# Kernel optimization log

Hardware: AMD Instinct MI355X
Metric: run time of the kernel (lower is better)

The kernel has to match this reference:

```python
import jax, jax.numpy as jnp
import numpy as np

N = 100000   # nodes
E = 600000   # edges
F = 128      # input features
H = 128      # hidden size
A = 64       # n_actions
G = 64       # number of graphs in batch
L = 3        # GAT layers
EPS = 1e-5   # GraphNorm eps


def setup_inputs() -> dict:
    key = jax.random.key(0)
    ks = jax.random.split(key, 8)
    x = jax.random.normal(ks[0], (N, F), dtype=jnp.float32)
    edge_index = jax.random.randint(ks[1], (2, E), 0, N, dtype=jnp.int64)
    batch = jnp.sort(jax.random.randint(ks[2], (N,), 0, G, dtype=jnp.int64))
    Ws = jax.random.normal(ks[3], (L, H, H), dtype=jnp.float32) * (1.0 / np.sqrt(H))
    att_src = jax.random.normal(ks[4], (L, H), dtype=jnp.float32) * 0.1
    att_dst = jax.random.normal(ks[5], (L, H), dtype=jnp.float32) * 0.1
    conv_bias = jnp.zeros((L, H), dtype=jnp.float32)
    gn_weight = jnp.ones((L - 1, H), dtype=jnp.float32)
    gn_bias = jnp.zeros((L - 1, H), dtype=jnp.float32)
    gn_mean_scale = jnp.ones((L - 1, H), dtype=jnp.float32)
    W1 = jax.random.normal(ks[6], (H, H), dtype=jnp.float32) * (1.0 / np.sqrt(H))
    b1 = jnp.zeros((H,), dtype=jnp.float32)
    W2 = jax.random.normal(ks[7], (H, A), dtype=jnp.float32) * (1.0 / np.sqrt(H))
    b2 = jnp.zeros((A,), dtype=jnp.float32)
    return dict(x=x, edge_index=edge_index, batch=batch, Ws=Ws, att_src=att_src,
                att_dst=att_dst, conv_bias=conv_bias, gn_weight=gn_weight,
                gn_bias=gn_bias, gn_mean_scale=gn_mean_scale,
                W1=W1, b1=b1, W2=W2, b2=b2)


def reference(x, edge_index, batch, Ws, att_src, att_dst, conv_bias,
              gn_weight, gn_bias, gn_mean_scale, W1, b1, W2, b2):
    src, dst = edge_index[0], edge_index[1]
    n = x.shape[0]
    h = x
    for l in range(L):
        # GATConv (heads=1, add_self_loops=False): h' = W h, edge attention
        hW = h @ Ws[l]                              # [N,H]
        a_s = hW @ att_src[l]                       # [N]
        a_d = hW @ att_dst[l]                       # [N]
        e = jax.nn.leaky_relu(a_s[src] + a_d[dst], 0.2)      # [E]
        m = jax.ops.segment_max(e, dst, num_segments=n)      # stable softmax per dst
        ex = jnp.exp(e - m[dst])
        s = jax.ops.segment_sum(ex, dst, num_segments=n)
        alpha = ex / (s[dst] + 1e-16)               # PyG softmax eps
        h = jax.ops.segment_sum(hW[src] * alpha[:, None], dst, num_segments=n) + conv_bias[l]
        if l < L - 1:
            # GraphNorm with batch=None (source passes no batch to gnn): one graph
            mean = h.mean(axis=0, keepdims=True)
            out = h - mean * gn_mean_scale[l]
            var = (out * out).mean(axis=0, keepdims=True)
            h = gn_weight[l] * out / jnp.sqrt(var + EPS) + gn_bias[l]
            h = jax.nn.leaky_relu(h, 0.01)          # act between layers (not after last)
    pooled = jax.ops.segment_sum(h, batch, num_segments=G)   # global_add_pool [G,H]
    z = jax.nn.leaky_relu(pooled @ W1 + b1, 0.01)
    return z @ W2 + b2                               # [G,A]
```

## Files before the change

kernel.cpp:

```cpp
#include <hip/hip_runtime.h>
#include <math.h>

#define HD 128
#define GG 64
#define CSB 256

typedef __attribute__((ext_vector_type(8))) short short8;
typedef __attribute__((ext_vector_type(4))) float f32x4;
typedef __attribute__((ext_vector_type(2))) float f32x2;

__device__ __forceinline__ float leaky(float x, float s) { return x > 0.f ? x : s * x; }

__device__ __forceinline__ unsigned short bf16_of(float f) {
    union { float f; unsigned u; } v; v.f = f;
    unsigned r = v.u + 0x7fffu + ((v.u >> 16) & 1u);
    return (unsigned short)(r >> 16);
}
__device__ __forceinline__ float f_of_bf16(unsigned short u) {
    union { unsigned u; float f; } v; v.u = ((unsigned)u) << 16;
    return v.f;
}

__device__ __forceinline__ int sw(int row, int chunk) {
    return row * 128 + ((chunk ^ (row & 15)) << 3);
}

__global__ void k_init(const float* __restrict__ Ws, unsigned short* __restrict__ Wt,
                       int* __restrict__ bcnt) {
    int i = blockIdx.x * 256 + threadIdx.x;
    if (i < 3 * 16384) {
        int l = i >> 14, rem = i & 16383;
        int nn = rem >> 7, k = rem & 127;
        Wt[i] = bf16_of(Ws[l * 16384 + k * 128 + nn]);
    }
    if (i < 513) bcnt[i] = 0;
}


__global__ __launch_bounds__(256) void k_gemm_a32(
    const float* __restrict__ A, const unsigned short* __restrict__ Wt,
    const float* __restrict__ att_s, const float* __restrict__ att_d,
    unsigned short* __restrict__ hWb, float* __restrict__ a_s, float* __restrict__ a_d,
    int n) {
    __shared__ unsigned short Bs[128 * 128];
    const int tid = threadIdx.x;
    const int base = blockIdx.x * 64;

    const uint4* Wt4 = (const uint4*)Wt;
    uint4* Bs4 = (uint4*)Bs;
#pragma unroll
    for (int j = 0; j < 8; ++j) {
        int flat = tid + j * 256;
        int col = flat >> 4, c8 = flat & 15;
        Bs4[(col << 4) + (c8 ^ (col & 15))] = Wt4[flat];
    }

    const int wave = tid >> 6, lane = tid & 63;
    const int m16 = lane & 15, quad = lane >> 4;

    short8 af[4];
    {
        int row = base + wave * 16 + m16;
        row = (row < n) ? row : (n - 1);
        const float4* ap = (const float4*)(A + (size_t)row * 128);
#pragma unroll
        for (int kk = 0; kk < 4; ++kk) {
            float4 v0 = ap[kk * 8 + quad * 2];
            float4 v1 = ap[kk * 8 + quad * 2 + 1];
            union { short8 s; unsigned u[4]; } P;
            P.u[0] = (unsigned)bf16_of(v0.x) | ((unsigned)bf16_of(v0.y) << 16);
            P.u[1] = (unsigned)bf16_of(v0.z) | ((unsigned)bf16_of(v0.w) << 16);
            P.u[2] = (unsigned)bf16_of(v1.x) | ((unsigned)bf16_of(v1.y) << 16);
            P.u[3] = (unsigned)bf16_of(v1.z) | ((unsigned)bf16_of(v1.w) << 16);
            af[kk] = P.s;
        }
    }
    __syncthreads();

    f32x4 acc[8];
#pragma unroll
    for (int ct = 0; ct < 8; ++ct) acc[ct] = (f32x4){0.f, 0.f, 0.f, 0.f};
#pragma unroll
    for (int kk = 0; kk < 4; ++kk) {
#pragma unroll
        for (int ct = 0; ct < 8; ++ct) {
            short8 bfr = *(const short8*)&Bs[sw(ct * 16 + m16, kk * 4 + quad)];
            acc[ct] = __builtin_amdgcn_mfma_f32_16x16x32_bf16(af[kk], bfr, acc[ct], 0, 0, 0);
        }
    }

#pragma unroll
    for (int reg = 0; reg < 4; ++reg) {
        int gr = base + wave * 16 + quad * 4 + reg;
        bool ok = gr < n;
        unsigned short* rowp = hWb + (size_t)gr * 128 + m16;
        float s = 0.f, dd = 0.f;
#pragma unroll
        for (int ct = 0; ct < 8; ++ct) {
            float v = acc[ct][reg];
            int col = ct * 16 + m16;
            if (ok) rowp[ct * 16] = bf16_of(v);
            s = fmaf(v, att_s[col], s);
            dd = fmaf(v, att_d[col], dd);
        }
#pragma unroll
        for (int off = 1; off < 16; off <<= 1) {
            s += __shfl_xor(s, off, 64);
            dd += __shfl_xor(dd, off, 64);
        }
        if (m16 == 0 && ok) { a_s[gr] = s; a_d[gr] = dd; }
    }
}

__global__ __launch_bounds__(256) void k_gemm_a16(
    const unsigned short* __restrict__ Ab, const unsigned short* __restrict__ Wt,
    const float* __restrict__ att_s, const float* __restrict__ att_d,
    const float* __restrict__ alpha, const float* __restrict__ beta,
    unsigned short* __restrict__ hWb, float* __restrict__ a_s, float* __restrict__ a_d,
    int n) {
    __shared__ unsigned short Bs[128 * 128];
    const int tid = threadIdx.x;
    const int base = blockIdx.x * 64;

    const uint4* Wt4 = (const uint4*)Wt;
    uint4* Bs4 = (uint4*)Bs;
#pragma unroll
    for (int j = 0; j < 8; ++j) {
        int flat = tid + j * 256;
        int col = flat >> 4, c8 = flat & 15;
        Bs4[(col << 4) + (c8 ^ (col & 15))] = Wt4[flat];
    }

    const int wave = tid >> 6, lane = tid & 63;
    const int m16 = lane & 15, quad = lane >> 4;
    const float4* al4 = (const float4*)alpha;
    const float4* be4 = (const float4*)beta;

    short8 af[4];
    {
        int row = base + wave * 16 + m16;
        row = (row < n) ? row : (n - 1);
        const uint4* ap = (const uint4*)(Ab + (size_t)row * 128);
#pragma unroll
        for (int kk = 0; kk < 4; ++kk) {
            uint4 raw = ap[kk * 4 + quad];
            int c4 = kk * 8 + quad * 2;
            float4 a0 = al4[c4], a1 = al4[c4 + 1];
            float4 b0 = be4[c4], b1 = be4[c4 + 1];
            float f0 = leaky(fmaf(f_of_bf16(raw.x & 0xffff), a0.x, b0.x), 0.01f);
            float f1 = leaky(fmaf(f_of_bf16(raw.x >> 16),    a0.y, b0.y), 0.01f);
            float f2 = leaky(fmaf(f_of_bf16(raw.y & 0xffff), a0.z, b0.z), 0.01f);
            float f3 = leaky(fmaf(f_of_bf16(raw.y >> 16),    a0.w, b0.w), 0.01f);
            float f4 = leaky(fmaf(f_of_bf16(raw.z & 0xffff), a1.x, b1.x), 0.01f);
            float f5 = leaky(fmaf(f_of_bf16(raw.z >> 16),    a1.y, b1.y), 0.01f);
            float f6 = leaky(fmaf(f_of_bf16(raw.w & 0xffff), a1.z, b1.z), 0.01f);
            float f7 = leaky(fmaf(f_of_bf16(raw.w >> 16),    a1.w, b1.w), 0.01f);
            union { short8 s; unsigned u[4]; } P;
            P.u[0] = (unsigned)bf16_of(f0) | ((unsigned)bf16_of(f1) << 16);
            P.u[1] = (unsigned)bf16_of(f2) | ((unsigned)bf16_of(f3) << 16);
            P.u[2] = (unsigned)bf16_of(f4) | ((unsigned)bf16_of(f5) << 16);
            P.u[3] = (unsigned)bf16_of(f6) | ((unsigned)bf16_of(f7) << 16);
            af[kk] = P.s;
        }
    }
    __syncthreads();

    f32x4 acc[8];
#pragma unroll
    for (int ct = 0; ct < 8; ++ct) acc[ct] = (f32x4){0.f, 0.f, 0.f, 0.f};
#pragma unroll
    for (int kk = 0; kk < 4; ++kk) {
#pragma unroll
        for (int ct = 0; ct < 8; ++ct) {
            short8 bfr = *(const short8*)&Bs[sw(ct * 16 + m16, kk * 4 + quad)];
            acc[ct] = __builtin_amdgcn_mfma_f32_16x16x32_bf16(af[kk], bfr, acc[ct], 0, 0, 0);
        }
    }

#pragma unroll
    for (int reg = 0; reg < 4; ++reg) {
        int gr = base + wave * 16 + quad * 4 + reg;
        bool ok = gr < n;
        unsigned short* rowp = hWb + (size_t)gr * 128 + m16;
        float s = 0.f, dd = 0.f;
#pragma unroll
        for (int ct = 0; ct < 8; ++ct) {
            float v = acc[ct][reg];
            int col = ct * 16 + m16;
            if (ok) rowp[ct * 16] = bf16_of(v);
            s = fmaf(v, att_s[col], s);
            dd = fmaf(v, att_d[col], dd);
        }
#pragma unroll
        for (int off = 1; off < 16; off <<= 1) {
            s += __shfl_xor(s, off, 64);
            dd += __shfl_xor(dd, off, 64);
        }
        if (m16 == 0 && ok) { a_s[gr] = s; a_d[gr] = dd; }
    }
}


__global__ __launch_bounds__(256) void k_bcount(const int* __restrict__ dst,
                                                int* __restrict__ bcnt, int e) {
    __shared__ int lh[512];
    const int tid = threadIdx.x;
    for (int t = tid; t < 512; t += 256) lh[t] = 0;
    __syncthreads();
    for (int i = blockIdx.x * 256 + tid; i < e; i += gridDim.x * 256)
        atomicAdd(&lh[dst[i] >> 9], 1);
    __syncthreads();
    for (int t = tid; t < 512; t += 256)
        if (lh[t]) atomicAdd(&bcnt[t], lh[t]);
}

__global__ void k_bscan(const int* __restrict__ bcnt, int* __restrict__ bbase,
                        int* __restrict__ bcur, int* __restrict__ offs,
                        int nbk, int n, int e) {
    __shared__ int s[512];
    int t = threadIdx.x;
    int v = (t < nbk) ? bcnt[t] : 0;
    s[t] = v;
    __syncthreads();
    for (int off = 1; off < 512; off <<= 1) {
        int u = (t >= off) ? s[t - off] : 0;
        __syncthreads();
        s[t] += u;
        __syncthreads();
    }
    if (t < nbk) { bbase[t] = s[t] - v; bcur[t] = s[t] - v; }
    if (t == 0) { bbase[nbk] = e; offs[n] = e; }
}

__global__ __launch_bounds__(256) void k_part(const int* __restrict__ src,
                                              const int* __restrict__ dst,
                                              int* __restrict__ bcur,
                                              int* __restrict__ ebuf, int e) {
    __shared__ int lh[512];
    __shared__ int lbase[512];
    const int tid = threadIdx.x;
    const int chunk = (e + gridDim.x - 1) / gridDim.x;
    const int i0 = blockIdx.x * chunk;
    const int i1 = min(e, i0 + chunk);
    for (int t = tid; t < 512; t += 256) lh[t] = 0;
    __syncthreads();
    for (int i = i0 + tid; i < i1; i += 256) atomicAdd(&lh[dst[i] >> 9], 1);
    __syncthreads();
    for (int t = tid; t < 512; t += 256) {
        int c = lh[t];
        lbase[t] = c ? atomicAdd(&bcur[t], c) : 0;
    }
    __syncthreads();
    for (int t = tid; t < 512; t += 256) lh[t] = 0;
    __syncthreads();
    for (int i = i0 + tid; i < i1; i += 256) {
        int d = dst[i];
        int b = d >> 9;
        int p = lbase[b] + atomicAdd(&lh[b], 1);
        ebuf[p] = ((d & 511) << 18) | src[i];
    }
}

__global__ __launch_bounds__(256) void k_bscatter(const int* __restrict__ ebuf,
                                                  const int* __restrict__ bbase,
                                                  int* __restrict__ offs,
                                                  int* __restrict__ esrc, int n) {
    const int b = blockIdx.x;
    const int tid = threadIdx.x;
    const int nb0 = b << 9;
    const int e0 = bbase[b], e1 = bbase[b + 1];
    __shared__ int cnt[512];
    __shared__ int sc[512];
    __shared__ int pos[512];
    for (int t = tid; t < 512; t += 256) cnt[t] = 0;
    __syncthreads();
    for (int i = e0 + tid; i < e1; i += 256) atomicAdd(&cnt[ebuf[i] >> 18], 1);
    __syncthreads();
    for (int t = tid; t < 512; t += 256) sc[t] = cnt[t];
    __syncthreads();
    for (int off = 1; off < 512; off <<= 1) {
        int t0 = tid, t1 = tid + 256;
        int v0 = (t0 >= off) ? sc[t0 - off] : 0;
        int v1 = sc[t1 - off];
        __syncthreads();
        sc[t0] += v0;
        sc[t1] += v1;
        __syncthreads();
    }
    for (int t = tid; t < 512; t += 256) pos[t] = e0 + sc[t] - cnt[t];
    __syncthreads();
    for (int t = tid; t < 512; t += 256) {
        int node = nb0 + t;
        if (node < n) offs[node] = pos[t];
    }
    __syncthreads();
    for (int i = e0 + tid; i < e1; i += 256) {
        int v = ebuf[i];
        int l = v >> 18;
        int p = atomicAdd(&pos[l], 1);
        esrc[p] = v & 0x3FFFF;
    }
}

__global__ __launch_bounds__(256) void k_agg(const unsigned short* __restrict__ hWb,
                                             const int* __restrict__ offs,
                                             const int* __restrict__ esrc,
                                             const float* __restrict__ a_s,
                                             const float* __restrict__ a_d,
                                             const float* __restrict__ bias,
                                             unsigned short* __restrict__ hb, int n) {
    const int tid = threadIdx.x;
    const int l16 = tid & 15;
    const int d = blockIdx.x * 16 + (tid >> 4);
    if (d >= n) return;
    const int p0 = offs[d], p1 = offs[d + 1];
    const float ad = a_d[d];
    const uint4* hW8 = (const uint4*)hWb;

    f32x2 acc0 = {0.f, 0.f}, acc1 = {0.f, 0.f}, acc2 = {0.f, 0.f}, acc3 = {0.f, 0.f};
    float ssum = 0.f;

    int s_cur = (p0 < p1) ? esrc[p0] : 0;
    uint4 raw = hW8[(size_t)s_cur * 16 + l16];
    float as_cur = a_s[s_cur];
    for (int p = p0; p < p1; ++p) {
        const uint4 r = raw;
        const float e = leaky(as_cur + ad, 0.2f);
        const int pn = (p + 1 < p1) ? p + 1 : p;
        const int s_nxt = esrc[pn];
        raw = hW8[(size_t)s_nxt * 16 + l16];
        as_cur = a_s[s_nxt];

        const float ex = __expf(e);
        ssum += ex;
        const f32x2 exv = {ex, ex};
        f32x2 v;
        v.x = f_of_bf16(r.x & 0xffff); v.y = f_of_bf16(r.x >> 16);
        acc0 = __builtin_elementwise_fma(exv, v, acc0);
        v.x = f_of_bf16(r.y & 0xffff); v.y = f_of_bf16(r.y >> 16);
        acc1 = __builtin_elementwise_fma(exv, v, acc1);
        v.x = f_of_bf16(r.z & 0xffff); v.y = f_of_bf16(r.z >> 16);
        acc2 = __builtin_elementwise_fma(exv, v, acc2);
        v.x = f_of_bf16(r.w & 0xffff); v.y = f_of_bf16(r.w >> 16);
        acc3 = __builtin_elementwise_fma(exv, v, acc3);
    }

    const float inv = 1.f / (ssum + 1e-16f);
    const float4* b4p = (const float4*)bias;
    const float4 bb0 = b4p[l16 * 2], bb1 = b4p[l16 * 2 + 1];
    uint4 o;
    o.x = (unsigned)bf16_of(fmaf(acc0.x, inv, bb0.x)) |
          ((unsigned)bf16_of(fmaf(acc0.y, inv, bb0.y)) << 16);
    o.y = (unsigned)bf16_of(fmaf(acc1.x, inv, bb0.z)) |
          ((unsigned)bf16_of(fmaf(acc1.y, inv, bb0.w)) << 16);
    o.z = (unsigned)bf16_of(fmaf(acc2.x, inv, bb1.x)) |
          ((unsigned)bf16_of(fmaf(acc2.y, inv, bb1.y)) << 16);
    o.w = (unsigned)bf16_of(fmaf(acc3.x, inv, bb1.z)) |
          ((unsigned)bf16_of(fmaf(acc3.y, inv, bb1.w)) << 16);
    ((uint4*)hb)[(size_t)d * 16 + l16] = o;
}

__global__ __launch_bounds__(256) void k_colstat6(const unsigned short* __restrict__ hb,
                                                  float* __restrict__ part, int n) {
    const uint4* h8 = (const uint4*)hb;
    const int tid = threadIdx.x;
    const int total = n * 16;
    float s[8] = {0.f,0.f,0.f,0.f,0.f,0.f,0.f,0.f};
    float q[8] = {0.f,0.f,0.f,0.f,0.f,0.f,0.f,0.f};
    for (int i = blockIdx.x * 256 + tid; i < total; i += CSB * 256) {
        uint4 raw = h8[i];
        float v0 = f_of_bf16(raw.x & 0xffff), v1 = f_of_bf16(raw.x >> 16);
        float v2 = f_of_bf16(raw.y & 0xffff), v3 = f_of_bf16(raw.y >> 16);
        float v4 = f_of_bf16(raw.z & 0xffff), v5 = f_of_bf16(raw.z >> 16);
        float v6 = f_of_bf16(raw.w & 0xffff), v7 = f_of_bf16(raw.w >> 16);
        s[0] += v0; q[0] = fmaf(v0, v0, q[0]);
        s[1] += v1; q[1] = fmaf(v1, v1, q[1]);
        s[2] += v2; q[2] = fmaf(v2, v2, q[2]);
        s[3] += v3; q[3] = fmaf(v3, v3, q[3]);
        s[4] += v4; q[4] = fmaf(v4, v4, q[4]);
        s[5] += v5; q[5] = fmaf(v5, v5, q[5]);
        s[6] += v6; q[6] = fmaf(v6, v6, q[6]);
        s[7] += v7; q[7] = fmaf(v7, v7, q[7]);
    }
    __shared__ float ss[256][9];
    __shared__ float sq[256][9];
#pragma unroll
    for (int k = 0; k < 8; ++k) { ss[tid][k] = s[k]; sq[tid][k] = q[k]; }
    __syncthreads();
    if (tid < 128) {
        int c = tid >> 3, k = tid & 7;
        float S = 0.f, Q = 0.f;
#pragma unroll
        for (int g = 0; g < 16; ++g) {
            S += ss[g * 16 + c][k];
            Q += sq[g * 16 + c][k];
        }
        part[blockIdx.x * 256 + tid] = S;
        part[blockIdx.x * 256 + 128 + tid] = Q;
    }
}

__global__ __launch_bounds__(256) void k_colfin(const float* __restrict__ part,
                                                const float* __restrict__ w,
                                                const float* __restrict__ bb,
                                                const float* __restrict__ ms,
                                                float* __restrict__ alpha,
                                                float* __restrict__ beta, float inv_n) {
    int tid = threadIdx.x;
    float a0 = 0.f, a1 = 0.f, a2 = 0.f, a3 = 0.f;
    for (int b = 0; b < CSB; b += 4) {
        a0 += part[(b + 0) * 256 + tid];
        a1 += part[(b + 1) * 256 + tid];
        a2 += part[(b + 2) * 256 + tid];
        a3 += part[(b + 3) * 256 + tid];
    }
    __shared__ float fin[256];
    fin[tid] = (a0 + a1) + (a2 + a3);
    __syncthreads();
    if (tid < 128) {
        float mean = fin[tid] * inv_n;
        float ex2 = fin[128 + tid] * inv_n;
        float m2 = mean * ms[tid];
        float var = ex2 - 2.f * m2 * mean + m2 * m2;
        float a = w[tid] * rsqrtf(var + 1e-5f);
        alpha[tid] = a;
        beta[tid] = bb[tid] - m2 * a;
    }
}

__device__ __forceinline__ int lower_bound_i(const int* __restrict__ a, int n, int key) {
    int lo = 0, hi = n;
    while (lo < hi) {
        int mid = (lo + hi) >> 1;
        if (a[mid] < key) lo = mid + 1; else hi = mid;
    }
    return lo;
}

__global__ __launch_bounds__(256) void k_pool(const unsigned short* __restrict__ hb,
                                              const int* __restrict__ batch,
                                              float* __restrict__ pooled4, int n) {
    int g = blockIdx.x >> 2, t4 = blockIdx.x & 3;
    int lo = lower_bound_i(batch, n, g);
    int hi = lower_bound_i(batch, n, g + 1);
    int len = hi - lo;
    int q = (len + 3) >> 2;
    int r0 = lo + t4 * q;
    int r1 = min(r0 + q, hi);
    int c4 = threadIdx.x & 31, rg = threadIdx.x >> 5;
    const ushort4* h4 = (const ushort4*)hb;
    float4 acc = make_float4(0.f, 0.f, 0.f, 0.f);
    for (int r = r0 + rg; r < r1; r += 8) {
        ushort4 hv = h4[(size_t)r * 32 + c4];
        acc.x += f_of_bf16(hv.x);
        acc.y += f_of_bf16(hv.y);
        acc.z += f_of_bf16(hv.z);
        acc.w += f_of_bf16(hv.w);
    }
    __shared__ float4 sred[256];
    sred[threadIdx.x] = acc;
    __syncthreads();
    if (threadIdx.x < 32) {
        float4 S = sred[threadIdx.x];
#pragma unroll
        for (int k = 1; k < 8; ++k) {
            float4 a = sred[threadIdx.x + 32 * k];
            S.x += a.x; S.y += a.y; S.z += a.z; S.w += a.w;
        }
        ((float4*)pooled4)[(t4 * GG + g) * 32 + threadIdx.x] = S;
    }
}

__global__ __launch_bounds__(128) void k_mlp(const float* __restrict__ pooled4,
                                             const float* __restrict__ W1,
                                             const float* __restrict__ b1,
                                             const float* __restrict__ W2,
                                             const float* __restrict__ b2,
                                             float* __restrict__ out) {
    __shared__ float pr[HD];
    __shared__ float zs[HD];
    int g = blockIdx.x, t = threadIdx.x;
    float pv = 0.f;
#pragma unroll
    for (int k = 0; k < 4; ++k) pv += pooled4[(k * GG + g) * HD + t];
    pr[t] = pv;
    __syncthreads();
    float acc = b1[t];
#pragma unroll 8
    for (int k = 0; k < HD; ++k) acc = fmaf(pr[k], W1[k * HD + t], acc);
    zs[t] = leaky(acc, 0.01f);
    __syncthreads();
    if (t < 64) {
        float a2 = b2[t];
#pragma unroll 8
        for (int k = 0; k < HD; ++k) a2 = fmaf(zs[k], W2[k * 64 + t], a2);
        out[g * 64 + t] = a2;
    }
}

extern "C" void kernel_launch(void* const* d_in, const int* in_sizes, int n_in,
                              void* d_out, int out_size, void* d_ws, size_t ws_size,
                              hipStream_t stream) {
    const float* x        = (const float*)d_in[0];
    const int*   ei       = (const int*)d_in[1];
    const int*   batch    = (const int*)d_in[2];
    const float* Ws       = (const float*)d_in[3];
    const float* att_src  = (const float*)d_in[4];
    const float* att_dst  = (const float*)d_in[5];
    const float* conv_bias= (const float*)d_in[6];
    const float* gn_w     = (const float*)d_in[7];
    const float* gn_b     = (const float*)d_in[8];
    const float* gn_ms    = (const float*)d_in[9];
    const float* W1       = (const float*)d_in[10];
    const float* b1       = (const float*)d_in[11];
    const float* W2       = (const float*)d_in[12];
    const float* b2       = (const float*)d_in[13];
    float* out = (float*)d_out;

    const int n = in_sizes[2];
    const int e = in_sizes[1] / 2;
    const int* src = ei;
    const int* dst = ei + e;
    const int nbk = (n + 511) >> 9;

    char* ws = (char*)d_ws;
    unsigned short* hWb = (unsigned short*)ws;
    unsigned short* hb  = hWb + (size_t)n * HD;
    float* a_s    = (float*)(hb + (size_t)n * HD);
    float* a_d    = a_s + n;
    float* alpha  = a_d + n;
    float* beta   = alpha + HD;
    float* pooled4= beta + HD;
    float* part   = pooled4 + 4 * GG * HD;
    unsigned short* Wt = (unsigned short*)(part + CSB * 256);
    int* offs     = (int*)(Wt + 3 * 16384);
    int* esrc     = offs + n + 1;
    int* ebuf     = esrc + e;
    int* bcnt     = ebuf + e;
    int* bbase    = bcnt + 513;
    int* bcur     = bbase + 514;

    k_init<<<192, 256, 0, stream>>>(Ws, Wt, bcnt);
    k_bcount<<<256, 256, 0, stream>>>(dst, bcnt, e);
    k_bscan<<<1, 512, 0, stream>>>(bcnt, bbase, bcur, offs, nbk, n, e);
    k_part<<<256, 256, 0, stream>>>(src, dst, bcur, ebuf, e);
    k_bscatter<<<nbk, 256, 0, stream>>>(ebuf, bbase, offs, esrc, n);

    for (int l = 0; l < 3; ++l) {
        if (l == 0) {
            k_gemm_a32<<<(n + 63) / 64, 256, 0, stream>>>(
                x, Wt, att_src, att_dst, hWb, a_s, a_d, n);
        } else {
            k_gemm_a16<<<(n + 63) / 64, 256, 0, stream>>>(
                hb, Wt + l * 16384, att_src + l * HD, att_dst + l * HD,
                alpha, beta, hWb, a_s, a_d, n);
        }
        k_agg<<<(n + 15) / 16, 256, 0, stream>>>(hWb, offs, esrc, a_s, a_d,
                                                 conv_bias + l * HD, hb, n);
        if (l < 2) {
            k_colstat6<<<CSB, 256, 0, stream>>>(hb, part, n);
            k_colfin<<<1, 256, 0, stream>>>(part, gn_w + l * HD, gn_b + l * HD,
                                            gn_ms + l * HD, alpha, beta, 1.0f / n);
        }
    }

    k_pool<<<4 * GG, 256, 0, stream>>>(hb, batch, pooled4, n);
    k_mlp<<<GG, HD, 0, stream>>>(pooled4, W1, b1, W2, b2, out);
}
```

Before: 357.6 us.

## Sort destination nodes by degree for aggregation and transpose MFMA epilogue

Adds a counting sort of destination nodes by in-degree (histogram, scan, scatter into a permutation), and the aggregation kernel now walks nodes in that order. Nodes with similar edge counts then share a wavefront, which is meant to reduce divergence and idle lanes. Separately, the GEMM swaps the MFMA operands so each lane holds four consecutive columns of one row. The epilogue can then write packed 8-byte bf16 stores and compute the attention dot products with fewer shuffles. The price is three extra small kernels plus an indirection through perm, and hb writes lose locality because nodes are processed in degree order.

```diff
diff --git a/kernel.cpp b/kernel.cpp
--- a/kernel.cpp
+++ b/kernel.cpp
@@ -26,7 +26,7 @@
 }
 
 __global__ void k_init(const float* __restrict__ Ws, unsigned short* __restrict__ Wt,
-                       int* __restrict__ bcnt) {
+                       int* __restrict__ bcnt, int* __restrict__ dcnt) {
     int i = blockIdx.x * 256 + threadIdx.x;
     if (i < 3 * 16384) {
         int l = i >> 14, rem = i & 16383;
@@ -34,6 +34,7 @@
         Wt[i] = bf16_of(Ws[l * 16384 + k * 128 + nn]);
     }
     if (i < 513) bcnt[i] = 0;
+    if (i < 128) dcnt[i] = 0;
 }
 
 
@@ -85,30 +86,36 @@
 #pragma unroll
         for (int ct = 0; ct < 8; ++ct) {
             short8 bfr = *(const short8*)&Bs[sw(ct * 16 + m16, kk * 4 + quad)];
-            acc[ct] = __builtin_amdgcn_mfma_f32_16x16x32_bf16(af[kk], bfr, acc[ct], 0, 0, 0);
-        }
-    }
-
-#pragma unroll
-    for (int reg = 0; reg < 4; ++reg) {
-        int gr = base + wave * 16 + quad * 4 + reg;
-        bool ok = gr < n;
-        unsigned short* rowp = hWb + (size_t)gr * 128 + m16;
+            acc[ct] = __builtin_amdgcn_mfma_f32_16x16x32_bf16(bfr, af[kk], acc[ct], 0, 0, 0);
+        }
+    }
+
+    {
+        int row = base + wave * 16 + m16;
+        bool ok = row < n;
+        unsigned short* rowp = hWb + (size_t)row * 128 + quad * 4;
+        const float4* as4 = (const float4*)att_s;
+        const float4* ad4 = (const float4*)att_d;
         float s = 0.f, dd = 0.f;
 #pragma unroll
         for (int ct = 0; ct < 8; ++ct) {
-            float v = acc[ct][reg];
-            int col = ct * 16 + m16;
-            if (ok) rowp[ct * 16] = bf16_of(v);
-            s = fmaf(v, att_s[col], s);
-            dd = fmaf(v, att_d[col], dd);
-        }
-#pragma unroll
-        for (int off = 1; off < 16; off <<= 1) {
-            s += __shfl_xor(s, off, 64);
-            dd += __shfl_xor(dd, off, 64);
-        }
-        if (m16 == 0 && ok) { a_s[gr] = s; a_d[gr] = dd; }
+            f32x4 a = acc[ct];
+            float4 As = as4[ct * 4 + quad];
+            float4 Ad = ad4[ct * 4 + quad];
+            s  = fmaf(a[0], As.x, fmaf(a[1], As.y, fmaf(a[2], As.z, fmaf(a[3], As.w, s))));
+            dd = fmaf(a[0], Ad.x, fmaf(a[1], Ad.y, fmaf(a[2], Ad.z, fmaf(a[3], Ad.w, dd))));
+            if (ok) {
+                uint2 o;
+                o.x = (unsigned)bf16_of(a[0]) | ((unsigned)bf16_of(a[1]) << 16);
+                o.y = (unsigned)bf16_of(a[2]) | ((unsigned)bf16_of(a[3]) << 16);
+                *(uint2*)(rowp + ct * 16) = o;
+            }
+        }
+        s  += __shfl_xor(s, 16, 64);
+        s  += __shfl_xor(s, 32, 64);
+        dd += __shfl_xor(dd, 16, 64);
+        dd += __shfl_xor(dd, 32, 64);
+        if (ok && quad == 0) { a_s[row] = s; a_d[row] = dd; }
     }
 }
 
@@ -173,30 +180,36 @@
 #pragma unroll
         for (int ct = 0; ct < 8; ++ct) {
             short8 bfr = *(const short8*)&Bs[sw(ct * 16 + m16, kk * 4 + quad)];
-            acc[ct] = __builtin_amdgcn_mfma_f32_16x16x32_bf16(af[kk], bfr, acc[ct], 0, 0, 0);
-        }
-    }
-
-#pragma unroll
-    for (int reg = 0; reg < 4; ++reg) {
-        int gr = base + wave * 16 + quad * 4 + reg;
-        bool ok = gr < n;
-        unsigned short* rowp = hWb + (size_t)gr * 128 + m16;
+            acc[ct] = __builtin_amdgcn_mfma_f32_16x16x32_bf16(bfr, af[kk], acc[ct], 0, 0, 0);
+        }
+    }
+
+    {
+        int row = base + wave * 16 + m16;
+        bool ok = row < n;
+        unsigned short* rowp = hWb + (size_t)row * 128 + quad * 4;
+        const float4* as4 = (const float4*)att_s;
+        const float4* ad4 = (const float4*)att_d;
         float s = 0.f, dd = 0.f;
 #pragma unroll
         for (int ct = 0; ct < 8; ++ct) {
-            float v = acc[ct][reg];
-            int col = ct * 16 + m16;
-            if (ok) rowp[ct * 16] = bf16_of(v);
-            s = fmaf(v, att_s[col], s);
-            dd = fmaf(v, att_d[col], dd);
-        }
-#pragma unroll
-        for (int off = 1; off < 16; off <<= 1) {
-            s += __shfl_xor(s, off, 64);
-            dd += __shfl_xor(dd, off, 64);
-        }
-        if (m16 == 0 && ok) { a_s[gr] = s; a_d[gr] = dd; }
+            f32x4 a = acc[ct];
+            float4 As = as4[ct * 4 + quad];
+            float4 Ad = ad4[ct * 4 + quad];
+            s  = fmaf(a[0], As.x, fmaf(a[1], As.y, fmaf(a[2], As.z, fmaf(a[3], As.w, s))));
+            dd = fmaf(a[0], Ad.x, fmaf(a[1], Ad.y, fmaf(a[2], Ad.z, fmaf(a[3], Ad.w, dd))));
+            if (ok) {
+                uint2 o;
+                o.x = (unsigned)bf16_of(a[0]) | ((unsigned)bf16_of(a[1]) << 16);
+                o.y = (unsigned)bf16_of(a[2]) | ((unsigned)bf16_of(a[3]) << 16);
+                *(uint2*)(rowp + ct * 16) = o;
+            }
+        }
+        s  += __shfl_xor(s, 16, 64);
+        s  += __shfl_xor(s, 32, 64);
+        dd += __shfl_xor(dd, 16, 64);
+        dd += __shfl_xor(dd, 32, 64);
+        if (ok && quad == 0) { a_s[row] = s; a_d[row] = dd; }
     }
 }
 
@@ -302,17 +315,78 @@
     }
 }
 
+__global__ __launch_bounds__(256) void k_dhist(const int* __restrict__ offs,
+                                               int* __restrict__ dcnt, int n) {
+    __shared__ int lh[128];
+    const int tid = threadIdx.x;
+    if (tid < 128) lh[tid] = 0;
+    __syncthreads();
+    for (int i = blockIdx.x * 256 + tid; i < n; i += gridDim.x * 256) {
+        int deg = offs[i + 1] - offs[i];
+        atomicAdd(&lh[min(deg, 127)], 1);
+    }
+    __syncthreads();
+    if (tid < 128 && lh[tid]) atomicAdd(&dcnt[tid], lh[tid]);
+}
+
+__global__ void k_dscan(const int* __restrict__ dcnt, int* __restrict__ dcur) {
+    __shared__ int s[128];
+    int t = threadIdx.x;
+    int v = dcnt[t];
+    s[t] = v;
+    __syncthreads();
+    for (int off = 1; off < 128; off <<= 1) {
+        int u = (t >= off) ? s[t - off] : 0;
+        __syncthreads();
+        s[t] += u;
+        __syncthreads();
+    }
+    dcur[t] = s[t] - v;
+}
+
+__global__ __launch_bounds__(256) void k_dscatter(const int* __restrict__ offs,
+                                                  int* __restrict__ dcur,
+                                                  int* __restrict__ perm, int n) {
+    __shared__ int lh[128];
+    __shared__ int lbase[128];
+    const int tid = threadIdx.x;
+    const int chunk = (n + gridDim.x - 1) / gridDim.x;
+    const int i0 = blockIdx.x * chunk;
+    const int i1 = min(n, i0 + chunk);
+    if (tid < 128) lh[tid] = 0;
+    __syncthreads();
+    for (int i = i0 + tid; i < i1; i += 256) {
+        int deg = offs[i + 1] - offs[i];
+        atomicAdd(&lh[min(deg, 127)], 1);
+    }
+    __syncthreads();
+    if (tid < 128) {
+        int c = lh[tid];
+        lbase[tid] = c ? atomicAdd(&dcur[tid], c) : 0;
+    }
+    __syncthreads();
+    if (tid < 128) lh[tid] = 0;
+    __syncthreads();
+    for (int i = i0 + tid; i < i1; i += 256) {
+        int b = min(offs[i + 1] - offs[i], 127);
+        int p = lbase[b] + atomicAdd(&lh[b], 1);
+        perm[p] = i;
+    }
+}
+
 __global__ __launch_bounds__(256) void k_agg(const unsigned short* __restrict__ hWb,
                                              const int* __restrict__ offs,
                                              const int* __restrict__ esrc,
+                                             const int* __restrict__ perm,
                                              const float* __restrict__ a_s,
                                              const float* __restrict__ a_d,
                                              const float* __restrict__ bias,
                                              unsigned short* __restrict__ hb, int n) {
     const int tid = threadIdx.x;
     const int l16 = tid & 15;
-    const int d = blockIdx.x * 16 + (tid >> 4);
-    if (d >= n) return;
+    const int g = blockIdx.x * 16 + (tid >> 4);
+    if (g >= n) return;
+    const int d = perm[g];
     const int p0 = offs[d], p1 = offs[d + 1];
     const float ad = a_d[d];
     const uint4* hW8 = (const uint4*)hWb;
@@ -539,12 +613,18 @@
     int* bcnt     = ebuf + e;
     int* bbase    = bcnt + 513;
     int* bcur     = bbase + 514;
-
-    k_init<<<192, 256, 0, stream>>>(Ws, Wt, bcnt);
+    int* perm     = bcur + 513;
+    int* dcnt     = perm + n;
+    int* dcur     = dcnt + 128;
+
+    k_init<<<192, 256, 0, stream>>>(Ws, Wt, bcnt, dcnt);
     k_bcount<<<256, 256, 0, stream>>>(dst, bcnt, e);
     k_bscan<<<1, 512, 0, stream>>>(bcnt, bbase, bcur, offs, nbk, n, e);
     k_part<<<256, 256, 0, stream>>>(src, dst, bcur, ebuf, e);
     k_bscatter<<<nbk, 256, 0, stream>>>(ebuf, bbase, offs, esrc, n);
+    k_dhist<<<128, 256, 0, stream>>>(offs, dcnt, n);
+    k_dscan<<<1, 128, 0, stream>>>(dcnt, dcur);
+    k_dscatter<<<128, 256, 0, stream>>>(offs, dcur, perm, n);
 
     for (int l = 0; l < 3; ++l) {
         if (l == 0) {
@@ -555,7 +635,7 @@
                 hb, Wt + l * 16384, att_src + l * HD, att_dst + l * HD,
                 alpha, beta, hWb, a_s, a_d, n);
         }
-        k_agg<<<(n + 15) / 16, 256, 0, stream>>>(hWb, offs, esrc, a_s, a_d,
+        k_agg<<<(n + 15) / 16, 256, 0, stream>>>(hWb, offs, esrc, perm, a_s, a_d,
                                                  conv_bias + l * HD, hb, n);
         if (l < 2) {
             k_colstat6<<<CSB, 256, 0, stream>>>(hb, part, n);
```

Result: slower. 381.6 us (+6.7%).

## Fuse GraphNorm column statistics into the aggregation kernel via atomic partials

Applied to the files above, without the earlier changes.

Each aggregation block now reduces the per-column sum and sum of squares of its output rows in shared memory. It then atomically adds them into one of 256 partial slots, so the separate k_colstat6 pass that re-read the whole hidden matrix is removed. Two zeroed partial buffers, one per normalized layer, are cleared in k_init. This saves one full read of the bf16 node features per layer and one launch. In exchange k_agg uses more shared memory and does float atomics. The statistics are taken from fp32 values before bf16 rounding, which changes them slightly.

```diff
diff --git a/kernel.cpp b/kernel.cpp
--- a/kernel.cpp
+++ b/kernel.cpp
@@ -26,7 +26,7 @@
 }
 
 __global__ void k_init(const float* __restrict__ Ws, unsigned short* __restrict__ Wt,
-                       int* __restrict__ bcnt) {
+                       int* __restrict__ bcnt, float* __restrict__ part) {
     int i = blockIdx.x * 256 + threadIdx.x;
     if (i < 3 * 16384) {
         int l = i >> 14, rem = i & 16383;
@@ -34,6 +34,7 @@
         Wt[i] = bf16_of(Ws[l * 16384 + k * 128 + nn]);
     }
     if (i < 513) bcnt[i] = 0;
+    part[i] = 0.f;
 }
 
 
@@ -308,95 +309,86 @@
                                              const float* __restrict__ a_s,
                                              const float* __restrict__ a_d,
                                              const float* __restrict__ bias,
-                                             unsigned short* __restrict__ hb, int n) {
+                                             unsigned short* __restrict__ hb,
+                                             float* __restrict__ part, int n) {
+    __shared__ float ss[256][9];
+    __shared__ float sq[256][9];
     const int tid = threadIdx.x;
     const int l16 = tid & 15;
     const int d = blockIdx.x * 16 + (tid >> 4);
-    if (d >= n) return;
-    const int p0 = offs[d], p1 = offs[d + 1];
-    const float ad = a_d[d];
-    const uint4* hW8 = (const uint4*)hWb;
+    const bool active = d < n;
 
     f32x2 acc0 = {0.f, 0.f}, acc1 = {0.f, 0.f}, acc2 = {0.f, 0.f}, acc3 = {0.f, 0.f};
     float ssum = 0.f;
-
-    int s_cur = (p0 < p1) ? esrc[p0] : 0;
-    uint4 raw = hW8[(size_t)s_cur * 16 + l16];
-    float as_cur = a_s[s_cur];
-    for (int p = p0; p < p1; ++p) {
-        const uint4 r = raw;
-        const float e = leaky(as_cur + ad, 0.2f);
-        const int pn = (p + 1 < p1) ? p + 1 : p;
-        const int s_nxt = esrc[pn];
-        raw = hW8[(size_t)s_nxt * 16 + l16];
-        as_cur = a_s[s_nxt];
-
-        const float ex = __expf(e);
-        ssum += ex;
-        const f32x2 exv = {ex, ex};
-        f32x2 v;
-        v.x = f_of_bf16(r.x & 0xffff); v.y = f_of_bf16(r.x >> 16);
-        acc0 = __builtin_elementwise_fma(exv, v, acc0);
-        v.x = f_of_bf16(r.y & 0xffff); v.y = f_of_bf16(r.y >> 16);
-        acc1 = __builtin_elementwise_fma(exv, v, acc1);
-        v.x = f_of_bf16(r.z & 0xffff); v.y = f_of_bf16(r.z >> 16);
-        acc2 = __builtin_elementwise_fma(exv, v, acc2);
-        v.x = f_of_bf16(r.w & 0xffff); v.y = f_of_bf16(r.w >> 16);
-        acc3 = __builtin_elementwise_fma(exv, v, acc3);
-    }
-
-    const float inv = 1.f / (ssum + 1e-16f);
-    const float4* b4p = (const float4*)bias;
-    const float4 bb0 = b4p[l16 * 2], bb1 = b4p[l16 * 2 + 1];
-    uint4 o;
-    o.x = (unsigned)bf16_of(fmaf(acc0.x, inv, bb0.x)) |
-          ((unsigned)bf16_of(fmaf(acc0.y, inv, bb0.y)) << 16);
-    o.y = (unsigned)bf16_of(fmaf(acc1.x, inv, bb0.z)) |
-          ((unsigned)bf16_of(fmaf(acc1.y, inv, bb0.w)) << 16);
-    o.z = (unsigned)bf16_of(fmaf(acc2.x, inv, bb1.x)) |
-          ((unsigned)bf16_of(fmaf(acc2.y, inv, bb1.y)) << 16);
-    o.w = (unsigned)bf16_of(fmaf(acc3.x, inv, bb1.z)) |
-          ((unsigned)bf16_of(fmaf(acc3.y, inv, bb1.w)) << 16);
-    ((uint4*)hb)[(size_t)d * 16 + l16] = o;
-}
-
-__global__ __launch_bounds__(256) void k_colstat6(const unsigned short* __restrict__ hb,
-                                                  float* __restrict__ part, int n) {
-    const uint4* h8 = (const uint4*)hb;
-    const int tid = threadIdx.x;
-    const int total = n * 16;
-    float s[8] = {0.f,0.f,0.f,0.f,0.f,0.f,0.f,0.f};
-    float q[8] = {0.f,0.f,0.f,0.f,0.f,0.f,0.f,0.f};
-    for (int i = blockIdx.x * 256 + tid; i < total; i += CSB * 256) {
-        uint4 raw = h8[i];
-        float v0 = f_of_bf16(raw.x & 0xffff), v1 = f_of_bf16(raw.x >> 16);
-        float v2 = f_of_bf16(raw.y & 0xffff), v3 = f_of_bf16(raw.y >> 16);
-        float v4 = f_of_bf16(raw.z & 0xffff), v5 = f_of_bf16(raw.z >> 16);
-        float v6 = f_of_bf16(raw.w & 0xffff), v7 = f_of_bf16(raw.w >> 16);
-        s[0] += v0; q[0] = fmaf(v0, v0, q[0]);
-        s[1] += v1; q[1] = fmaf(v1, v1, q[1]);
-        s[2] += v2; q[2] = fmaf(v2, v2, q[2]);
-        s[3] += v3; q[3] = fmaf(v3, v3, q[3]);
-        s[4] += v4; q[4] = fmaf(v4, v4, q[4]);
-        s[5] += v5; q[5] = fmaf(v5, v5, q[5]);
-        s[6] += v6; q[6] = fmaf(v6, v6, q[6]);
-        s[7] += v7; q[7] = fmaf(v7, v7, q[7]);
-    }
-    __shared__ float ss[256][9];
-    __shared__ float sq[256][9];
-#pragma unroll
-    for (int k = 0; k < 8; ++k) { ss[tid][k] = s[k]; sq[tid][k] = q[k]; }
-    __syncthreads();
-    if (tid < 128) {
-        int c = tid >> 3, k = tid & 7;
-        float S = 0.f, Q = 0.f;
-#pragma unroll
-        for (int g = 0; g < 16; ++g) {
-            S += ss[g * 16 + c][k];
-            Q += sq[g * 16 + c][k];
-        }
-        part[blockIdx.x * 256 + tid] = S;
-        part[blockIdx.x * 256 + 128 + tid] = Q;
+    float h0 = 0.f, h1 = 0.f, h2 = 0.f, h3 = 0.f, h4 = 0.f, h5 = 0.f, h6 = 0.f, h7 = 0.f;
+
+    if (active) {
+        const int p0 = offs[d], p1 = offs[d + 1];
+        const float ad = a_d[d];
+        const uint4* hW8 = (const uint4*)hWb;
+
+        int s_cur = (p0 < p1) ? esrc[p0] : 0;
+        uint4 raw = hW8[(size_t)s_cur * 16 + l16];
+        float as_cur = a_s[s_cur];
+        for (int p = p0; p < p1; ++p) {
+            const uint4 r = raw;
+            const float e = leaky(as_cur + ad, 0.2f);
+            const int pn = (p + 1 < p1) ? p + 1 : p;
+            const int s_nxt = esrc[pn];
+            raw = hW8[(size_t)s_nxt * 16 + l16];
+            as_cur = a_s[s_nxt];
+
+            const float ex = __expf(e);
+            ssum += ex;
+            const f32x2 exv = {ex, ex};
+            f32x2 v;
+            v.x = f_of_bf16(r.x & 0xffff); v.y = f_of_bf16(r.x >> 16);
+            acc0 = __builtin_elementwise_fma(exv, v, acc0);
+            v.x = f_of_bf16(r.y & 0xffff); v.y = f_of_bf16(r.y >> 16);
+            acc1 = __builtin_elementwise_fma(exv, v, acc1);
+            v.x = f_of_bf16(r.z & 0xffff); v.y = f_of_bf16(r.z >> 16);
+            acc2 = __builtin_elementwise_fma(exv, v, acc2);
+            v.x = f_of_bf16(r.w & 0xffff); v.y = f_of_bf16(r.w >> 16);
+            acc3 = __builtin_elementwise_fma(exv, v, acc3);
+        }
+
+        const float inv = 1.f / (ssum + 1e-16f);
+        const float4* b4p = (const float4*)bias;
+        const float4 bb0 = b4p[l16 * 2], bb1 = b4p[l16 * 2 + 1];
+        h0 = fmaf(acc0.x, inv, bb0.x); h1 = fmaf(acc0.y, inv, bb0.y);
+        h2 = fmaf(acc1.x, inv, bb0.z); h3 = fmaf(acc1.y, inv, bb0.w);
+        h4 = fmaf(acc2.x, inv, bb1.x); h5 = fmaf(acc2.y, inv, bb1.y);
+        h6 = fmaf(acc3.x, inv, bb1.z); h7 = fmaf(acc3.y, inv, bb1.w);
+        uint4 o;
+        o.x = (unsigned)bf16_of(h0) | ((unsigned)bf16_of(h1) << 16);
+        o.y = (unsigned)bf16_of(h2) | ((unsigned)bf16_of(h3) << 16);
+        o.z = (unsigned)bf16_of(h4) | ((unsigned)bf16_of(h5) << 16);
+        o.w = (unsigned)bf16_of(h6) | ((unsigned)bf16_of(h7) << 16);
+        ((uint4*)hb)[(size_t)d * 16 + l16] = o;
+    }
+
+    if (part != nullptr) {
+        ss[tid][0] = active ? h0 : 0.f; sq[tid][0] = active ? h0 * h0 : 0.f;
+        ss[tid][1] = active ? h1 : 0.f; sq[tid][1] = active ? h1 * h1 : 0.f;
+        ss[tid][2] = active ? h2 : 0.f; sq[tid][2] = active ? h2 * h2 : 0.f;
+        ss[tid][3] = active ? h3 : 0.f; sq[tid][3] = active ? h3 * h3 : 0.f;
+        ss[tid][4] = active ? h4 : 0.f; sq[tid][4] = active ? h4 * h4 : 0.f;
+        ss[tid][5] = active ? h5 : 0.f; sq[tid][5] = active ? h5 * h5 : 0.f;
+        ss[tid][6] = active ? h6 : 0.f; sq[tid][6] = active ? h6 * h6 : 0.f;
+        ss[tid][7] = active ? h7 : 0.f; sq[tid][7] = active ? h7 * h7 : 0.f;
+        __syncthreads();
+        if (tid < 128) {
+            int c = tid >> 3, k = tid & 7;
+            float S = 0.f, Q = 0.f;
+#pragma unroll
+            for (int g = 0; g < 16; ++g) {
+                S += ss[g * 16 + c][k];
+                Q += sq[g * 16 + c][k];
+            }
+            float* pslot = part + (size_t)(blockIdx.x & (CSB - 1)) * 256;
+            atomicAdd(&pslot[tid], S);
+            atomicAdd(&pslot[128 + tid], Q);
+        }
     }
 }
 
@@ -532,7 +524,7 @@
     float* beta   = alpha + HD;
     float* pooled4= beta + HD;
     float* part   = pooled4 + 4 * GG * HD;
-    unsigned short* Wt = (unsigned short*)(part + CSB * 256);
+    unsigned short* Wt = (unsigned short*)(part + 2 * CSB * 256);
     int* offs     = (int*)(Wt + 3 * 16384);
     int* esrc     = offs + n + 1;
     int* ebuf     = esrc + e;
@@ -540,7 +532,10 @@
     int* bbase    = bcnt + 513;
     int* bcur     = bbase + 514;
 
-    k_init<<<192, 256, 0, stream>>>(Ws, Wt, bcnt);
+    float* part0 = part;
+    float* part1 = part + CSB * 256;
+
+    k_init<<<512, 256, 0, stream>>>(Ws, Wt, bcnt, part);
     k_bcount<<<256, 256, 0, stream>>>(dst, bcnt, e);
     k_bscan<<<1, 512, 0, stream>>>(bcnt, bbase, bcur, offs, nbk, n, e);
     k_part<<<256, 256, 0, stream>>>(src, dst, bcur, ebuf, e);
@@ -555,11 +550,11 @@
                 hb, Wt + l * 16384, att_src + l * HD, att_dst + l * HD,
                 alpha, beta, hWb, a_s, a_d, n);
         }
+        float* lpart = (l == 0) ? part0 : (l == 1) ? part1 : nullptr;
         k_agg<<<(n + 15) / 16, 256, 0, stream>>>(hWb, offs, esrc, a_s, a_d,
-                                                 conv_bias + l * HD, hb, n);
+                                                 conv_bias + l * HD, hb, lpart, n);
         if (l < 2) {
-            k_colstat6<<<CSB, 256, 0, stream>>>(hb, part, n);
-            k_colfin<<<1, 256, 0, stream>>>(part, gn_w + l * HD, gn_b + l * HD,
+            k_colfin<<<1, 256, 0, stream>>>(lpart, gn_w + l * HD, gn_b + l * HD,
                                             gn_ms + l * HD, alpha, beta, 1.0f / n);
         }
     }
```

New measurement: 354.3 us. No clear change (-0.9%).
